# Kernel tuning notes

Hardware: AMD Instinct MI355X
Metric: run time of the kernel (lower is better)

Reference implementation:

```python
import jax, jax.numpy as jnp
import numpy as np

B, T, IN = 64, 1024, 512
H1, H2 = 64, 6

def _mk(key, shape, scale):
    return jax.random.uniform(key, shape, jnp.float32, -scale, scale)

def setup_inputs() -> dict:
    key = jax.random.key(0)
    ks = jax.random.split(key, 16)
    x = jax.random.normal(ks[0], (B, T, IN), jnp.float32)
    s1 = 1.0 / np.sqrt(H1)
    s2 = 1.0 / np.sqrt(H2)
    return {
        "x": x,
        # lstm1 (input 512 -> 64), 2 layers; bias = b_ih + b_hh folded together
        "w1_ih0": _mk(ks[1], (4 * H1, IN), s1), "w1_hh0": _mk(ks[2], (4 * H1, H1), s1), "b1_0": _mk(ks[3], (4 * H1,), s1),
        "w1_ih1": _mk(ks[4], (4 * H1, H1), s1), "w1_hh1": _mk(ks[5], (4 * H1, H1), s1), "b1_1": _mk(ks[6], (4 * H1,), s1),
        # lstm2 (64 -> 6), 2 layers
        "w2_ih0": _mk(ks[7], (4 * H2, H1), s2), "w2_hh0": _mk(ks[8], (4 * H2, H2), s2), "b2_0": _mk(ks[9], (4 * H2,), s2),
        "w2_ih1": _mk(ks[10], (4 * H2, H2), s2), "w2_hh1": _mk(ks[11], (4 * H2, H2), s2), "b2_1": _mk(ks[12], (4 * H2,), s2),
        # fc 6 -> 6
        "fc_w": _mk(ks[13], (H2, H2), s2), "fc_b": _mk(ks[14], (H2,), s2),
    }

def _lstm_layer(x, w_ih, w_hh, b):
    # x: [B, T, D]; w_ih: [4H, D]; w_hh: [4H, H]; b: [4H]
    H = w_hh.shape[1]
    xg = jnp.einsum('btd,gd->btg', x, w_ih) + b          # precompute input gates [B,T,4H]
    xg = jnp.transpose(xg, (1, 0, 2))                    # [T, B, 4H]
    h0 = jnp.zeros((x.shape[0], H), x.dtype)
    c0 = jnp.zeros((x.shape[0], H), x.dtype)

    def step(carry, g_t):
        h, c = carry
        gates = g_t + h @ w_hh.T                         # [B, 4H]
        i, f, g, o = jnp.split(gates, 4, axis=-1)        # pytorch gate order i,f,g,o
        i = jax.nn.sigmoid(i); f = jax.nn.sigmoid(f)
        g = jnp.tanh(g); o = jax.nn.sigmoid(o)
        c = f * c + i * g
        h = o * jnp.tanh(c)
        return (h, c), h

    _, hs = jax.lax.scan(step, (h0, c0), xg)             # hs: [T, B, H]
    return jnp.transpose(hs, (1, 0, 2))                  # [B, T, H]

def reference(x, w1_ih0, w1_hh0, b1_0, w1_ih1, w1_hh1, b1_1,
              w2_ih0, w2_hh0, b2_0, w2_ih1, w2_hh1, b2_1, fc_w, fc_b):
    h = _lstm_layer(x, w1_ih0, w1_hh0, b1_0)
    h = _lstm_layer(h, w1_ih1, w1_hh1, b1_1)
    h = _lstm_layer(h, w2_ih0, w2_hh0, b2_0)
    h = _lstm_layer(h, w2_ih1, w2_hh1, b2_1)
    return h @ fc_w.T + fc_b                             # [B, T, 6]
```

## Files before the change

kernel.cpp:

```cpp
#include <hip/hip_runtime.h>
#include <hip/hip_bf16.h>


#define B_SZ 64
#define T_SZ 1024
#define M_SZ (B_SZ * T_SZ)
#define CHUNK 16
#define PF 4

typedef _Float16 h2   __attribute__((ext_vector_type(2)));
typedef _Float16 h8   __attribute__((ext_vector_type(8)));
typedef float    f32x4 __attribute__((ext_vector_type(4)));

__device__ __forceinline__ float sigm_f(float x) {
    return 1.0f / (1.0f + __expf(-x));
}
__device__ __forceinline__ float tanh_f(float x) {
    return 2.0f / (1.0f + __expf(-2.0f * x)) - 1.0f;
}

__device__ __forceinline__ float fdot2f(h2 a, h2 b, float c) {
#if __has_builtin(__builtin_amdgcn_fdot2)
    return __builtin_amdgcn_fdot2(a, b, c, false);
#else
    return c + (float)a.x * (float)b.x + (float)a.y * (float)b.y;
#endif
}

__device__ __forceinline__ unsigned pack_h2(float a, float b) {
    h2 p; p.x = (_Float16)a; p.y = (_Float16)b;
    return __builtin_bit_cast(unsigned, p);
}
__device__ __forceinline__ h2 as_h2(unsigned x) { return __builtin_bit_cast(h2, x); }
__device__ __forceinline__ float as_f(unsigned x) { return __builtin_bit_cast(float, x); }
__device__ __forceinline__ float as_f(int x) { return __builtin_bit_cast(float, x); }

__device__ __forceinline__ int pack_pair(float h) {
    const _Float16 hf = (_Float16)h;
    const int hb = (int)__builtin_bit_cast(unsigned short, hf);
    const int nb = __builtin_amdgcn_update_dpp(0, hb, 0xB1, 0xF, 0xF, true);
    return hb | (nb << 16);
}

__device__ __forceinline__ void lstm_cell(float p0, float p1, float p2, float p3,
                                          float& c, float& h) {
    const float iv = sigm_f(p0);
    const float fv = sigm_f(p1);
    const float gv = tanh_f(p2);
    const float ov = sigm_f(p3);
    c = fv * c + iv * gv;
    h = ov * tanh_f(c);
}

__device__ __forceinline__ void wait_flag(const unsigned* f, unsigned need) {
    while (__hip_atomic_load(f, __ATOMIC_RELAXED, __HIP_MEMORY_SCOPE_AGENT) < need)
        __builtin_amdgcn_s_sleep(2);
    (void)__hip_atomic_load(f, __ATOMIC_ACQUIRE, __HIP_MEMORY_SCOPE_AGENT);
}
__device__ __forceinline__ void publish_flag(unsigned* f, unsigned v) {
    __hip_atomic_store(f, v, __ATOMIC_RELEASE, __HIP_MEMORY_SCOPE_AGENT);
}

__global__ __launch_bounds__(256) void f32_to_f16(const float* __restrict__ src,
                                                  _Float16* __restrict__ dst, int n) {
    const int i = blockIdx.x * 256 + threadIdx.x;
    if (i < n) dst[i] = (_Float16)src[i];
}

__global__ void init_flags(unsigned* f) { f[threadIdx.x] = 0; }

template <int K>
__global__ __launch_bounds__(256) void gemm_mfma(const float* __restrict__ X,
                                                 const _Float16* __restrict__ W16,
                                                 const float* __restrict__ bias,
                                                 float* __restrict__ out) {
    const int m0   = blockIdx.x * 64;
    const int tid  = threadIdx.x;
    const int wv   = tid >> 6;
    const int lane = tid & 63;
    const int lh   = lane & 15;
    const int quad = lane >> 4;
    const int n0   = wv * 64;

    __shared__ __align__(16) _Float16 Als[64 * 32];

    f32x4 acc[4][4];
#pragma unroll
    for (int nt = 0; nt < 4; ++nt) {
        const float bg = bias[n0 + nt * 16 + lh];
#pragma unroll
        for (int mt = 0; mt < 4; ++mt) {
            acc[mt][nt].x = bg; acc[mt][nt].y = bg;
            acc[mt][nt].z = bg; acc[mt][nt].w = bg;
        }
    }

    const int srow = tid >> 2;
    const int sk8  = tid & 3;
    const int sdst = srow * 32 + ((sk8 ^ (srow & 3)) * 8);

    for (int k0 = 0; k0 < K; k0 += 32) {
        const float* xr = X + (size_t)(m0 + srow) * K + k0 + sk8 * 8;
        const float4 a4 = ((const float4*)xr)[0];
        const float4 b4 = ((const float4*)xr)[1];
        h8 bfrag[4];
#pragma unroll
        for (int nt = 0; nt < 4; ++nt) {
            bfrag[nt] = *(const h8*)&W16[(size_t)(n0 + nt * 16 + lh) * K + k0 + quad * 8];
        }
        h8 hv;
        hv[0] = (_Float16)a4.x; hv[1] = (_Float16)a4.y;
        hv[2] = (_Float16)a4.z; hv[3] = (_Float16)a4.w;
        hv[4] = (_Float16)b4.x; hv[5] = (_Float16)b4.y;
        hv[6] = (_Float16)b4.z; hv[7] = (_Float16)b4.w;

        __syncthreads();
        *(h8*)&Als[sdst] = hv;
        __syncthreads();

        h8 afrag[4];
#pragma unroll
        for (int mt = 0; mt < 4; ++mt) {
            const int row = mt * 16 + lh;
            afrag[mt] = *(const h8*)&Als[row * 32 + ((quad ^ (row & 3)) * 8)];
        }
#pragma unroll
        for (int mt = 0; mt < 4; ++mt)
#pragma unroll
            for (int nt = 0; nt < 4; ++nt)
                acc[mt][nt] = __builtin_amdgcn_mfma_f32_16x16x32_f16(
                    afrag[mt], bfrag[nt], acc[mt][nt], 0, 0, 0);
    }

#pragma unroll
    for (int mt = 0; mt < 4; ++mt)
#pragma unroll
        for (int nt = 0; nt < 4; ++nt)
#pragma unroll
            for (int r = 0; r < 4; ++r)
                out[(size_t)(m0 + mt * 16 + quad * 4 + r) * 256 + n0 + nt * 16 + lh] =
                    acc[mt][nt][r];
}

__global__ __launch_bounds__(256, 1) void lstm_pipe(
        const float* __restrict__ xg,
        const float* __restrict__ whh1,
        const float* __restrict__ wih2,
        const float* __restrict__ whh2,
        const float* __restrict__ b2v,
        const float* __restrict__ wih3,
        const float* __restrict__ whh3,
        const float* __restrict__ b3v,
        const float* __restrict__ wih4,
        const float* __restrict__ whh4,
        const float* __restrict__ b4v,
        const float* __restrict__ fcw,
        const float* __restrict__ fcb,
        unsigned* __restrict__ h1p,
        float* __restrict__ h2g,
        unsigned* __restrict__ flags,
        float* __restrict__ out) {
    const int role = blockIdx.x >> 6;
    const int b    = blockIdx.x & 63;
    const int tid  = threadIdx.x;
    const int g    = tid >> 6;
    const int u    = tid & 63;

    __shared__ __align__(16) float pls[2][4][64];

    if (role == 0) {
        unsigned w[32];
        {
            const float* wr = whh1 + (size_t)(g * 64 + u) * 64;
#pragma unroll
            for (int k2 = 0; k2 < 32; ++k2) w[k2] = pack_h2(wr[2 * k2], wr[2 * k2 + 1]);
        }
        const float* xgb = xg + (size_t)b * T_SZ * 256 + g * 64 + u;
        float xv[4];
#pragma unroll
        for (int s = 0; s < 4; ++s) xv[s] = xgb[(size_t)s * 256];
        unsigned* hp = h1p + (size_t)b * T_SZ * 32;
        unsigned* fl = flags + b;
        float c = 0.0f, h = 0.0f;
        int pkS = 0;

        for (int t4 = 0; t4 < T_SZ; t4 += 4) {
#pragma unroll
            for (int s = 0; s < 4; ++s) {
                const int t = t4 + s;
                float a0 = xv[s], a1 = 0.f, a2 = 0.f, a3 = 0.f;
#pragma unroll
                for (int k8 = 0; k8 < 8; ++k8) {
                    const int hs0 = __builtin_amdgcn_readlane(pkS, 8 * k8 + 0);
                    const int hs1 = __builtin_amdgcn_readlane(pkS, 8 * k8 + 2);
                    const int hs2 = __builtin_amdgcn_readlane(pkS, 8 * k8 + 4);
                    const int hs3 = __builtin_amdgcn_readlane(pkS, 8 * k8 + 6);
                    a0 = fdot2f(as_h2(w[4 * k8 + 0]), __builtin_bit_cast(h2, hs0), a0);
                    a1 = fdot2f(as_h2(w[4 * k8 + 1]), __builtin_bit_cast(h2, hs1), a1);
                    a2 = fdot2f(as_h2(w[4 * k8 + 2]), __builtin_bit_cast(h2, hs2), a2);
                    a3 = fdot2f(as_h2(w[4 * k8 + 3]), __builtin_bit_cast(h2, hs3), a3);
                }
                pls[t & 1][g][u] = (a0 + a1) + (a2 + a3);
                asm volatile("s_waitcnt lgkmcnt(0)" ::: "memory");
                __builtin_amdgcn_s_barrier();
                asm volatile("" ::: "memory");
                const float p0 = pls[t & 1][0][u];
                const float p1 = pls[t & 1][1][u];
                const float p2 = pls[t & 1][2][u];
                const float p3 = pls[t & 1][3][u];
                const int tp = (t + 4 < T_SZ) ? (t + 4) : (T_SZ - 1);
                xv[s] = xgb[(size_t)tp * 256];
                lstm_cell(p0, p1, p2, p3, c, h);
                pkS = pack_pair(h);
                if (g == 0) {
                    if (!(u & 1)) hp[(size_t)t * 32 + (u >> 1)] = (unsigned)pkS;
                    if (u == 0 && ((t & (CHUNK - 1)) == (CHUNK - 1)))
                        publish_flag(fl, (unsigned)(t + 1));
                }
            }
        }
    } else if (role == 1) {
        unsigned wi[32], wh[32];
        {
            const float* a = wih2 + (size_t)(g * 64 + u) * 64;
            const float* bb = whh2 + (size_t)(g * 64 + u) * 64;
#pragma unroll
            for (int k2 = 0; k2 < 32; ++k2) {
                wi[k2] = pack_h2(a[2 * k2], a[2 * k2 + 1]);
                wh[k2] = pack_h2(bb[2 * k2], bb[2 * k2 + 1]);
            }
        }
        const float bias = b2v[g * 64 + u];
        const unsigned* hp = h1p + (size_t)b * T_SZ * 32;
        float* h2b = h2g + (size_t)b * T_SZ * 64;
        unsigned* flin  = flags + b;
        unsigned* flout = flags + 64 + b;

        wait_flag(flin, (T_SZ < CHUNK + PF) ? T_SZ : (CHUNK + PF));
        unsigned hv[4];
#pragma unroll
        for (int s = 0; s < 4; ++s) hv[s] = hp[(size_t)s * 32 + (u & 31)];
        float c = 0.0f, h = 0.0f;
        int pkQ = 0;

        for (int t4 = 0; t4 < T_SZ; t4 += 4) {
            if (t4 && (t4 & (CHUNK - 1)) == 0) {
                unsigned need = t4 + CHUNK + PF;
                if (need > T_SZ) need = T_SZ;
                wait_flag(flin, need);
            }
#pragma unroll
            for (int s = 0; s < 4; ++s) {
                const int t = t4 + s;
                const int hw = (int)hv[s];
                float a0 = bias, a1 = 0.f, a2 = 0.f, a3 = 0.f;
                float d0 = 0.f, d1 = 0.f, d2 = 0.f, d3 = 0.f;
#pragma unroll
                for (int k8 = 0; k8 < 8; ++k8) {
                    const int j = 4 * k8;
                    const int i0 = __builtin_amdgcn_readlane(hw, j + 0);
                    const int i1 = __builtin_amdgcn_readlane(hw, j + 1);
                    const int i2 = __builtin_amdgcn_readlane(hw, j + 2);
                    const int i3 = __builtin_amdgcn_readlane(hw, j + 3);
                    a0 = fdot2f(as_h2(wi[j + 0]), __builtin_bit_cast(h2, i0), a0);
                    a1 = fdot2f(as_h2(wi[j + 1]), __builtin_bit_cast(h2, i1), a1);
                    a2 = fdot2f(as_h2(wi[j + 2]), __builtin_bit_cast(h2, i2), a2);
                    a3 = fdot2f(as_h2(wi[j + 3]), __builtin_bit_cast(h2, i3), a3);
                    const int q0 = __builtin_amdgcn_readlane(pkQ, 2 * j + 0);
                    const int q1 = __builtin_amdgcn_readlane(pkQ, 2 * j + 2);
                    const int q2 = __builtin_amdgcn_readlane(pkQ, 2 * j + 4);
                    const int q3 = __builtin_amdgcn_readlane(pkQ, 2 * j + 6);
                    d0 = fdot2f(as_h2(wh[j + 0]), __builtin_bit_cast(h2, q0), d0);
                    d1 = fdot2f(as_h2(wh[j + 1]), __builtin_bit_cast(h2, q1), d1);
                    d2 = fdot2f(as_h2(wh[j + 2]), __builtin_bit_cast(h2, q2), d2);
                    d3 = fdot2f(as_h2(wh[j + 3]), __builtin_bit_cast(h2, q3), d3);
                }
                pls[t & 1][g][u] = ((a0 + a1) + (a2 + a3)) + ((d0 + d1) + (d2 + d3));
                asm volatile("s_waitcnt lgkmcnt(0)" ::: "memory");
                __builtin_amdgcn_s_barrier();
                asm volatile("" ::: "memory");
                const float p0 = pls[t & 1][0][u];
                const float p1 = pls[t & 1][1][u];
                const float p2 = pls[t & 1][2][u];
                const float p3 = pls[t & 1][3][u];
                const int tp = (t + 4 < T_SZ) ? (t + 4) : (T_SZ - 1);
                hv[s] = hp[(size_t)tp * 32 + (u & 31)];
                lstm_cell(p0, p1, p2, p3, c, h);
                pkQ = pack_pair(h);
                if (g == 0) {
                    h2b[(size_t)t * 64 + u] = h;
                    if (u == 0 && ((t & (CHUNK - 1)) == (CHUNK - 1)))
                        publish_flag(flout, (unsigned)(t + 1));
                }
            }
        }
    } else {
        if (tid >= 64) return;
        float pw[64];
#pragma unroll
        for (int i = 0; i < 64; ++i) pw[i] = 0.0f;
        float pb = 0.0f;

        if (u < 6) {
#pragma unroll
            for (int g4 = 0; g4 < 4; ++g4)
#pragma unroll
                for (int k = 0; k < 6; ++k)
                    pw[g4 * 6 + k] = whh3[(g4 * 6 + u) * 6 + k];
        } else if (u < 12) {
            const int q = u - 6;
#pragma unroll
            for (int g4 = 0; g4 < 4; ++g4) {
#pragma unroll
                for (int k = 0; k < 6; ++k) {
                    pw[g4 * 6 + k]      = wih4[(g4 * 6 + q) * 6 + k];
                    pw[24 + g4 * 6 + k] = whh4[(g4 * 6 + q) * 6 + k];
                }
                pw[48 + g4] = b4v[g4 * 6 + q];
            }
        } else if (u < 18) {
            const int q = u - 12;
#pragma unroll
            for (int k = 0; k < 6; ++k) pw[52 + k] = fcw[q * 6 + k];
            pb = fcb[q];
        } else if (u >= 24 && u < 48) {
            const int q = u - 24;
#pragma unroll
            for (int j = 0; j < 64; ++j) pw[j] = wih3[(size_t)q * 64 + j];
            pb = b3v[q];
        }

        const float* h2b = h2g + (size_t)b * T_SZ * 64;
        unsigned* flin = flags + 64 + b;
        float* outb = out + (size_t)b * T_SZ * 6;

        wait_flag(flin, (T_SZ < CHUNK + PF) ? T_SZ : (CHUNK + PF));
        float hv[4];
#pragma unroll
        for (int s = 0; s < 4; ++s) hv[s] = h2b[(size_t)s * 64 + u];
        float c = 0.0f, h = 0.0f;
        const int bpa = 96 + (u % 6) * 4;

        for (int t4 = 0; t4 < T_SZ + 4; t4 += 4) {
            if (t4 && t4 < T_SZ && (t4 & (CHUNK - 1)) == 0) {
                unsigned need = t4 + CHUNK + PF;
                if (need > T_SZ) need = T_SZ;
                wait_flag(flin, need);
            }
#pragma unroll
            for (int s = 0; s < 4; ++s) {
                const int tt = t4 + s;
                const int hb = __builtin_bit_cast(int, h);
                float v3[6], v4[6];
#pragma unroll
                for (int k = 0; k < 6; ++k) v3[k] = as_f(__builtin_amdgcn_readlane(hb, k));
#pragma unroll
                for (int k = 0; k < 6; ++k) v4[k] = as_f(__builtin_amdgcn_readlane(hb, 6 + k));

                if (tt >= 2 && tt < T_SZ + 2 && u >= 12 && u < 18) {
                    float o = pb;
#pragma unroll
                    for (int k = 0; k < 6; ++k) o = fmaf(pw[52 + k], v4[k], o);
                    outb[(size_t)(tt - 2) * 6 + (u - 12)] = o;
                }
                if (tt >= 1 && tt <= T_SZ && u >= 6 && u < 12) {
                    float pg0 = pw[48], pg1 = pw[49], pg2 = pw[50], pg3 = pw[51];
#pragma unroll
                    for (int k = 0; k < 6; ++k) {
                        pg0 = fmaf(pw[0 * 6 + k], v3[k], pg0);
                        pg1 = fmaf(pw[1 * 6 + k], v3[k], pg1);
                        pg2 = fmaf(pw[2 * 6 + k], v3[k], pg2);
                        pg3 = fmaf(pw[3 * 6 + k], v3[k], pg3);
                        pg0 = fmaf(pw[24 + 0 * 6 + k], v4[k], pg0);
                        pg1 = fmaf(pw[24 + 1 * 6 + k], v4[k], pg1);
                        pg2 = fmaf(pw[24 + 2 * 6 + k], v4[k], pg2);
                        pg3 = fmaf(pw[24 + 3 * 6 + k], v4[k], pg3);
                    }
                    lstm_cell(pg0, pg1, pg2, pg3, c, h);
                }
                float pr = 0.0f;
                if (tt < T_SZ) {
                    const int hw = __builtin_bit_cast(int, hv[s]);
                    float d0 = pb, d1 = 0.f, d2 = 0.f, d3 = 0.f;
#pragma unroll
                    for (int j = 0; j < 64; j += 4) {
                        d0 = fmaf(pw[j + 0], as_f(__builtin_amdgcn_readlane(hw, j + 0)), d0);
                        d1 = fmaf(pw[j + 1], as_f(__builtin_amdgcn_readlane(hw, j + 1)), d1);
                        d2 = fmaf(pw[j + 2], as_f(__builtin_amdgcn_readlane(hw, j + 2)), d2);
                        d3 = fmaf(pw[j + 3], as_f(__builtin_amdgcn_readlane(hw, j + 3)), d3);
                    }
                    pr = (d0 + d1) + (d2 + d3);
                }
                const int prb = __builtin_bit_cast(int, pr);
                float pr4[4];
#pragma unroll
                for (int g4 = 0; g4 < 4; ++g4)
                    pr4[g4] = as_f(__builtin_amdgcn_ds_bpermute(bpa + g4 * 24, prb));
                if (tt < T_SZ) {
                    const int tp = (tt + 4 < T_SZ) ? (tt + 4) : (T_SZ - 1);
                    hv[s] = h2b[(size_t)tp * 64 + u];
                }
                if (tt < T_SZ && u < 6) {
                    float q0 = pr4[0], q1 = pr4[1], q2 = pr4[2], q3 = pr4[3];
#pragma unroll
                    for (int k = 0; k < 6; ++k) {
                        q0 = fmaf(pw[0 * 6 + k], v3[k], q0);
                        q1 = fmaf(pw[1 * 6 + k], v3[k], q1);
                        q2 = fmaf(pw[2 * 6 + k], v3[k], q2);
                        q3 = fmaf(pw[3 * 6 + k], v3[k], q3);
                    }
                    lstm_cell(q0, q1, q2, q3, c, h);
                }
            }
        }
    }
}

extern "C" void kernel_launch(void* const* d_in, const int* in_sizes, int n_in,
                              void* d_out, int out_size, void* d_ws, size_t ws_size,
                              hipStream_t stream) {
    const float* x      = (const float*)d_in[0];
    const float* w1_ih0 = (const float*)d_in[1];
    const float* w1_hh0 = (const float*)d_in[2];
    const float* b1_0   = (const float*)d_in[3];
    const float* w1_ih1 = (const float*)d_in[4];
    const float* w1_hh1 = (const float*)d_in[5];
    const float* b1_1   = (const float*)d_in[6];
    const float* w2_ih0 = (const float*)d_in[7];
    const float* w2_hh0 = (const float*)d_in[8];
    const float* b2_0   = (const float*)d_in[9];
    const float* w2_ih1 = (const float*)d_in[10];
    const float* w2_hh1 = (const float*)d_in[11];
    const float* b2_1   = (const float*)d_in[12];
    const float* fc_w   = (const float*)d_in[13];
    const float* fc_b   = (const float*)d_in[14];
    float* out = (float*)d_out;

    const int M = M_SZ;
    float*    xg    = (float*)d_ws;
    unsigned* h1p   = (unsigned*)(xg + (size_t)M * 256);
    float*    h2g   = (float*)(h1p + (size_t)M * 32);
    _Float16* w16a  = (_Float16*)(h2g + (size_t)M * 64);
    unsigned* flags = (unsigned*)(w16a + 256 * 512);

    init_flags<<<1, 128, 0, stream>>>(flags);
    f32_to_f16<<<(256 * 512 + 255) / 256, 256, 0, stream>>>(w1_ih0, w16a, 256 * 512);

    gemm_mfma<512><<<M / 64, 256, 0, stream>>>(x, w16a, b1_0, xg);

    lstm_pipe<<<192, 256, 0, stream>>>(xg, w1_hh0,
                                       w1_ih1, w1_hh1, b1_1,
                                       w2_ih0, w2_hh0, b2_0,
                                       w2_ih1, w2_hh1, b2_1,
                                       fc_w, fc_b,
                                       h1p, h2g, flags, out);
}
```

Before: 1.154 ms.

## Split LSTM input projections into separate pipelined block roles

The fused recurrent kernel is reorganized from three roles into five. Dedicated blocks now compute the layer-2 and layer-3 input projections chunk by chunk and hand them on through flags, with layer 2 writing in place into the already-consumed xg buffer and layer 3 using a new pr3 buffer. This takes the input matvecs off the serial per-timestep recurrence of the layer-2 and tail-layer blocks, so each recurrent step only does the hidden-state product. The cost is more blocks (320 instead of 192), which must all be co-resident for the spin-waits to work, plus extra global traffic and one more flag handoff adding pipeline latency.

```diff
diff --git a/kernel.cpp b/kernel.cpp
--- a/kernel.cpp
+++ b/kernel.cpp
@@ -143,7 +143,8 @@
 }
 
 __global__ __launch_bounds__(256, 1) void lstm_pipe(
-        const float* __restrict__ xg,
+        const float* __restrict__ xgc,
+        float* __restrict__ xgw,
         const float* __restrict__ whh1,
         const float* __restrict__ wih2,
         const float* __restrict__ whh2,
@@ -158,6 +159,7 @@
         const float* __restrict__ fcb,
         unsigned* __restrict__ h1p,
         float* __restrict__ h2g,
+        float* __restrict__ pr3,
         unsigned* __restrict__ flags,
         float* __restrict__ out) {
     const int role = blockIdx.x >> 6;
@@ -175,7 +177,7 @@
 #pragma unroll
             for (int k2 = 0; k2 < 32; ++k2) w[k2] = pack_h2(wr[2 * k2], wr[2 * k2 + 1]);
         }
-        const float* xgb = xg + (size_t)b * T_SZ * 256 + g * 64 + u;
+        const float* xgb = xgc + (size_t)b * T_SZ * 256 + g * 64 + u;
         float xv[4];
 #pragma unroll
         for (int s = 0; s < 4; ++s) xv[s] = xgb[(size_t)s * 256];
@@ -220,26 +222,61 @@
             }
         }
     } else if (role == 1) {
-        unsigned wi[32], wh[32];
+        unsigned wi[32];
         {
             const float* a = wih2 + (size_t)(g * 64 + u) * 64;
-            const float* bb = whh2 + (size_t)(g * 64 + u) * 64;
-#pragma unroll
-            for (int k2 = 0; k2 < 32; ++k2) {
-                wi[k2] = pack_h2(a[2 * k2], a[2 * k2 + 1]);
-                wh[k2] = pack_h2(bb[2 * k2], bb[2 * k2 + 1]);
-            }
-        }
-        const float bias = b2v[g * 64 + u];
+#pragma unroll
+            for (int k2 = 0; k2 < 32; ++k2) wi[k2] = pack_h2(a[2 * k2], a[2 * k2 + 1]);
+        }
+        const float breg = b2v[g * 64 + u];
         const unsigned* hp = h1p + (size_t)b * T_SZ * 32;
+        float* p2 = xgw + (size_t)b * T_SZ * 256 + g * 64 + u;
+        unsigned* fin  = flags + b;
+        unsigned* fout = flags + 64 + b;
+
+        for (int c0 = 0; c0 < T_SZ; c0 += CHUNK) {
+            wait_flag(fin, (unsigned)(c0 + CHUNK));
+            for (int tt = c0; tt < c0 + CHUNK; tt += 4) {
+                unsigned hv[4];
+#pragma unroll
+                for (int s = 0; s < 4; ++s) hv[s] = hp[(size_t)(tt + s) * 32 + (u & 31)];
+#pragma unroll
+                for (int s = 0; s < 4; ++s) {
+                    const int hw = (int)hv[s];
+                    float a0 = breg, a1 = 0.f, a2 = 0.f, a3 = 0.f;
+#pragma unroll
+                    for (int k8 = 0; k8 < 8; ++k8) {
+                        const int j = 4 * k8;
+                        const int i0 = __builtin_amdgcn_readlane(hw, j + 0);
+                        const int i1 = __builtin_amdgcn_readlane(hw, j + 1);
+                        const int i2 = __builtin_amdgcn_readlane(hw, j + 2);
+                        const int i3 = __builtin_amdgcn_readlane(hw, j + 3);
+                        a0 = fdot2f(as_h2(wi[j + 0]), __builtin_bit_cast(h2, i0), a0);
+                        a1 = fdot2f(as_h2(wi[j + 1]), __builtin_bit_cast(h2, i1), a1);
+                        a2 = fdot2f(as_h2(wi[j + 2]), __builtin_bit_cast(h2, i2), a2);
+                        a3 = fdot2f(as_h2(wi[j + 3]), __builtin_bit_cast(h2, i3), a3);
+                    }
+                    p2[(size_t)(tt + s) * 256] = (a0 + a1) + (a2 + a3);
+                }
+            }
+            publish_flag(fout, (unsigned)(c0 + CHUNK));
+        }
+    } else if (role == 2) {
+        unsigned wh[32];
+        {
+            const float* a = whh2 + (size_t)(g * 64 + u) * 64;
+#pragma unroll
+            for (int k2 = 0; k2 < 32; ++k2) wh[k2] = pack_h2(a[2 * k2], a[2 * k2 + 1]);
+        }
+        const float* p2 = xgc + (size_t)b * T_SZ * 256 + g * 64 + u;
         float* h2b = h2g + (size_t)b * T_SZ * 64;
-        unsigned* flin  = flags + b;
-        unsigned* flout = flags + 64 + b;
-
-        wait_flag(flin, (T_SZ < CHUNK + PF) ? T_SZ : (CHUNK + PF));
-        unsigned hv[4];
-#pragma unroll
-        for (int s = 0; s < 4; ++s) hv[s] = hp[(size_t)s * 32 + (u & 31)];
+        unsigned* fin  = flags + 64 + b;
+        unsigned* fout = flags + 128 + b;
+
+        wait_flag(fin, (T_SZ < CHUNK + PF) ? T_SZ : (CHUNK + PF));
+        float xv[4];
+#pragma unroll
+        for (int s = 0; s < 4; ++s) xv[s] = p2[(size_t)s * 256];
         float c = 0.0f, h = 0.0f;
         int pkQ = 0;
 
@@ -247,141 +284,68 @@
             if (t4 && (t4 & (CHUNK - 1)) == 0) {
                 unsigned need = t4 + CHUNK + PF;
                 if (need > T_SZ) need = T_SZ;
-                wait_flag(flin, need);
+                wait_flag(fin, need);
             }
 #pragma unroll
             for (int s = 0; s < 4; ++s) {
                 const int t = t4 + s;
-                const int hw = (int)hv[s];
-                float a0 = bias, a1 = 0.f, a2 = 0.f, a3 = 0.f;
-                float d0 = 0.f, d1 = 0.f, d2 = 0.f, d3 = 0.f;
+                float a0 = xv[s], a1 = 0.f, a2 = 0.f, a3 = 0.f;
 #pragma unroll
                 for (int k8 = 0; k8 < 8; ++k8) {
-                    const int j = 4 * k8;
-                    const int i0 = __builtin_amdgcn_readlane(hw, j + 0);
-                    const int i1 = __builtin_amdgcn_readlane(hw, j + 1);
-                    const int i2 = __builtin_amdgcn_readlane(hw, j + 2);
-                    const int i3 = __builtin_amdgcn_readlane(hw, j + 3);
-                    a0 = fdot2f(as_h2(wi[j + 0]), __builtin_bit_cast(h2, i0), a0);
-                    a1 = fdot2f(as_h2(wi[j + 1]), __builtin_bit_cast(h2, i1), a1);
-                    a2 = fdot2f(as_h2(wi[j + 2]), __builtin_bit_cast(h2, i2), a2);
-                    a3 = fdot2f(as_h2(wi[j + 3]), __builtin_bit_cast(h2, i3), a3);
-                    const int q0 = __builtin_amdgcn_readlane(pkQ, 2 * j + 0);
-                    const int q1 = __builtin_amdgcn_readlane(pkQ, 2 * j + 2);
-                    const int q2 = __builtin_amdgcn_readlane(pkQ, 2 * j + 4);
-                    const int q3 = __builtin_amdgcn_readlane(pkQ, 2 * j + 6);
-                    d0 = fdot2f(as_h2(wh[j + 0]), __builtin_bit_cast(h2, q0), d0);
-                    d1 = fdot2f(as_h2(wh[j + 1]), __builtin_bit_cast(h2, q1), d1);
-                    d2 = fdot2f(as_h2(wh[j + 2]), __builtin_bit_cast(h2, q2), d2);
-                    d3 = fdot2f(as_h2(wh[j + 3]), __builtin_bit_cast(h2, q3), d3);
-                }
-                pls[t & 1][g][u] = ((a0 + a1) + (a2 + a3)) + ((d0 + d1) + (d2 + d3));
+                    const int q0 = __builtin_amdgcn_readlane(pkQ, 8 * k8 + 0);
+                    const int q1 = __builtin_amdgcn_readlane(pkQ, 8 * k8 + 2);
+                    const int q2 = __builtin_amdgcn_readlane(pkQ, 8 * k8 + 4);
+                    const int q3 = __builtin_amdgcn_readlane(pkQ, 8 * k8 + 6);
+                    a0 = fdot2f(as_h2(wh[4 * k8 + 0]), __builtin_bit_cast(h2, q0), a0);
+                    a1 = fdot2f(as_h2(wh[4 * k8 + 1]), __builtin_bit_cast(h2, q1), a1);
+                    a2 = fdot2f(as_h2(wh[4 * k8 + 2]), __builtin_bit_cast(h2, q2), a2);
+                    a3 = fdot2f(as_h2(wh[4 * k8 + 3]), __builtin_bit_cast(h2, q3), a3);
+                }
+                pls[t & 1][g][u] = (a0 + a1) + (a2 + a3);
                 asm volatile("s_waitcnt lgkmcnt(0)" ::: "memory");
                 __builtin_amdgcn_s_barrier();
                 asm volatile("" ::: "memory");
                 const float p0 = pls[t & 1][0][u];
                 const float p1 = pls[t & 1][1][u];
-                const float p2 = pls[t & 1][2][u];
+                const float p2v = pls[t & 1][2][u];
                 const float p3 = pls[t & 1][3][u];
                 const int tp = (t + 4 < T_SZ) ? (t + 4) : (T_SZ - 1);
-                hv[s] = hp[(size_t)tp * 32 + (u & 31)];
-                lstm_cell(p0, p1, p2, p3, c, h);
+                xv[s] = p2[(size_t)tp * 256];
+                lstm_cell(p0, p1, p2v, p3, c, h);
                 pkQ = pack_pair(h);
                 if (g == 0) {
                     h2b[(size_t)t * 64 + u] = h;
                     if (u == 0 && ((t & (CHUNK - 1)) == (CHUNK - 1)))
-                        publish_flag(flout, (unsigned)(t + 1));
-                }
-            }
-        }
-    } else {
+                        publish_flag(fout, (unsigned)(t + 1));
+                }
+            }
+        }
+    } else if (role == 3) {
         if (tid >= 64) return;
         float pw[64];
 #pragma unroll
-        for (int i = 0; i < 64; ++i) pw[i] = 0.0f;
-        float pb = 0.0f;
-
-        if (u < 6) {
-#pragma unroll
-            for (int g4 = 0; g4 < 4; ++g4)
-#pragma unroll
-                for (int k = 0; k < 6; ++k)
-                    pw[g4 * 6 + k] = whh3[(g4 * 6 + u) * 6 + k];
-        } else if (u < 12) {
-            const int q = u - 6;
-#pragma unroll
-            for (int g4 = 0; g4 < 4; ++g4) {
-#pragma unroll
-                for (int k = 0; k < 6; ++k) {
-                    pw[g4 * 6 + k]      = wih4[(g4 * 6 + q) * 6 + k];
-                    pw[24 + g4 * 6 + k] = whh4[(g4 * 6 + q) * 6 + k];
-                }
-                pw[48 + g4] = b4v[g4 * 6 + q];
-            }
-        } else if (u < 18) {
-            const int q = u - 12;
-#pragma unroll
-            for (int k = 0; k < 6; ++k) pw[52 + k] = fcw[q * 6 + k];
-            pb = fcb[q];
-        } else if (u >= 24 && u < 48) {
-            const int q = u - 24;
-#pragma unroll
-            for (int j = 0; j < 64; ++j) pw[j] = wih3[(size_t)q * 64 + j];
-            pb = b3v[q];
-        }
-
+        for (int j = 0; j < 64; ++j) pw[j] = 0.0f;
+        float breg = 0.0f;
+        if (u < 24) {
+#pragma unroll
+            for (int j = 0; j < 64; ++j) pw[j] = wih3[(size_t)u * 64 + j];
+            breg = b3v[u];
+        }
         const float* h2b = h2g + (size_t)b * T_SZ * 64;
-        unsigned* flin = flags + 64 + b;
-        float* outb = out + (size_t)b * T_SZ * 6;
-
-        wait_flag(flin, (T_SZ < CHUNK + PF) ? T_SZ : (CHUNK + PF));
-        float hv[4];
-#pragma unroll
-        for (int s = 0; s < 4; ++s) hv[s] = h2b[(size_t)s * 64 + u];
-        float c = 0.0f, h = 0.0f;
-        const int bpa = 96 + (u % 6) * 4;
-
-        for (int t4 = 0; t4 < T_SZ + 4; t4 += 4) {
-            if (t4 && t4 < T_SZ && (t4 & (CHUNK - 1)) == 0) {
-                unsigned need = t4 + CHUNK + PF;
-                if (need > T_SZ) need = T_SZ;
-                wait_flag(flin, need);
-            }
-#pragma unroll
-            for (int s = 0; s < 4; ++s) {
-                const int tt = t4 + s;
-                const int hb = __builtin_bit_cast(int, h);
-                float v3[6], v4[6];
-#pragma unroll
-                for (int k = 0; k < 6; ++k) v3[k] = as_f(__builtin_amdgcn_readlane(hb, k));
-#pragma unroll
-                for (int k = 0; k < 6; ++k) v4[k] = as_f(__builtin_amdgcn_readlane(hb, 6 + k));
-
-                if (tt >= 2 && tt < T_SZ + 2 && u >= 12 && u < 18) {
-                    float o = pb;
-#pragma unroll
-                    for (int k = 0; k < 6; ++k) o = fmaf(pw[52 + k], v4[k], o);
-                    outb[(size_t)(tt - 2) * 6 + (u - 12)] = o;
-                }
-                if (tt >= 1 && tt <= T_SZ && u >= 6 && u < 12) {
-                    float pg0 = pw[48], pg1 = pw[49], pg2 = pw[50], pg3 = pw[51];
-#pragma unroll
-                    for (int k = 0; k < 6; ++k) {
-                        pg0 = fmaf(pw[0 * 6 + k], v3[k], pg0);
-                        pg1 = fmaf(pw[1 * 6 + k], v3[k], pg1);
-                        pg2 = fmaf(pw[2 * 6 + k], v3[k], pg2);
-                        pg3 = fmaf(pw[3 * 6 + k], v3[k], pg3);
-                        pg0 = fmaf(pw[24 + 0 * 6 + k], v4[k], pg0);
-                        pg1 = fmaf(pw[24 + 1 * 6 + k], v4[k], pg1);
-                        pg2 = fmaf(pw[24 + 2 * 6 + k], v4[k], pg2);
-                        pg3 = fmaf(pw[24 + 3 * 6 + k], v4[k], pg3);
-                    }
-                    lstm_cell(pg0, pg1, pg2, pg3, c, h);
-                }
-                float pr = 0.0f;
-                if (tt < T_SZ) {
+        float* prb = pr3 + (size_t)b * T_SZ * 24;
+        unsigned* fin  = flags + 128 + b;
+        unsigned* fout = flags + 192 + b;
+
+        for (int c0 = 0; c0 < T_SZ; c0 += CHUNK) {
+            wait_flag(fin, (unsigned)(c0 + CHUNK));
+            for (int tt = c0; tt < c0 + CHUNK; tt += 4) {
+                float hv[4];
+#pragma unroll
+                for (int s = 0; s < 4; ++s) hv[s] = h2b[(size_t)(tt + s) * 64 + u];
+#pragma unroll
+                for (int s = 0; s < 4; ++s) {
                     const int hw = __builtin_bit_cast(int, hv[s]);
-                    float d0 = pb, d1 = 0.f, d2 = 0.f, d3 = 0.f;
+                    float d0 = breg, d1 = 0.f, d2 = 0.f, d3 = 0.f;
 #pragma unroll
                     for (int j = 0; j < 64; j += 4) {
                         d0 = fmaf(pw[j + 0], as_f(__builtin_amdgcn_readlane(hw, j + 0)), d0);
@@ -389,28 +353,95 @@
                         d2 = fmaf(pw[j + 2], as_f(__builtin_amdgcn_readlane(hw, j + 2)), d2);
                         d3 = fmaf(pw[j + 3], as_f(__builtin_amdgcn_readlane(hw, j + 3)), d3);
                     }
-                    pr = (d0 + d1) + (d2 + d3);
-                }
-                const int prb = __builtin_bit_cast(int, pr);
-                float pr4[4];
-#pragma unroll
-                for (int g4 = 0; g4 < 4; ++g4)
-                    pr4[g4] = as_f(__builtin_amdgcn_ds_bpermute(bpa + g4 * 24, prb));
-                if (tt < T_SZ) {
-                    const int tp = (tt + 4 < T_SZ) ? (tt + 4) : (T_SZ - 1);
-                    hv[s] = h2b[(size_t)tp * 64 + u];
-                }
-                if (tt < T_SZ && u < 6) {
-                    float q0 = pr4[0], q1 = pr4[1], q2 = pr4[2], q3 = pr4[3];
-#pragma unroll
-                    for (int k = 0; k < 6; ++k) {
-                        q0 = fmaf(pw[0 * 6 + k], v3[k], q0);
-                        q1 = fmaf(pw[1 * 6 + k], v3[k], q1);
-                        q2 = fmaf(pw[2 * 6 + k], v3[k], q2);
-                        q3 = fmaf(pw[3 * 6 + k], v3[k], q3);
-                    }
-                    lstm_cell(q0, q1, q2, q3, c, h);
-                }
+                    if (u < 24) prb[(size_t)(tt + s) * 24 + u] = (d0 + d1) + (d2 + d3);
+                }
+            }
+            publish_flag(fout, (unsigned)(c0 + CHUNK));
+        }
+    } else {
+        if (tid >= 64) return;
+        float pw[48];
+#pragma unroll
+        for (int j = 0; j < 48; ++j) pw[j] = 0.0f;
+        float wf[7] = {0.f, 0.f, 0.f, 0.f, 0.f, 0.f, 0.f};
+        float wb[4] = {0.f, 0.f, 0.f, 0.f};
+        if (u < 6) {
+#pragma unroll
+            for (int g4 = 0; g4 < 4; ++g4)
+#pragma unroll
+                for (int k = 0; k < 6; ++k)
+                    pw[g4 * 12 + k] = whh3[(g4 * 6 + u) * 6 + k];
+        } else if (u < 12) {
+            const int q = u - 6;
+#pragma unroll
+            for (int g4 = 0; g4 < 4; ++g4) {
+#pragma unroll
+                for (int k = 0; k < 6; ++k) {
+                    pw[g4 * 12 + k]     = wih4[(g4 * 6 + q) * 6 + k];
+                    pw[g4 * 12 + 6 + k] = whh4[(g4 * 6 + q) * 6 + k];
+                }
+                wb[g4] = b4v[g4 * 6 + q];
+            }
+        } else if (u < 18) {
+            const int q = u - 12;
+#pragma unroll
+            for (int k = 0; k < 6; ++k) wf[k] = fcw[q * 6 + k];
+            wf[6] = fcb[q];
+        }
+        const float* prb = pr3 + (size_t)b * T_SZ * 24;
+        float* outb = out + (size_t)b * T_SZ * 6;
+        unsigned* fin = flags + 192 + b;
+        const int up  = (u < 24) ? u : 23;
+        const int bpa = ((u % 6) * 4);
+
+        wait_flag(fin, (T_SZ < CHUNK + PF) ? T_SZ : (CHUNK + PF));
+        float pf[4];
+#pragma unroll
+        for (int s = 0; s < 4; ++s) pf[s] = prb[(size_t)s * 24 + up];
+        float hS = 0.0f, cS = 0.0f;
+
+        for (int t4 = 0; t4 < T_SZ + 4; t4 += 4) {
+            if (t4 && t4 < T_SZ && (t4 & (CHUNK - 1)) == 0) {
+                unsigned need = t4 + CHUNK + PF;
+                if (need > T_SZ) need = T_SZ;
+                wait_flag(fin, need);
+            }
+#pragma unroll
+            for (int s = 0; s < 4; ++s) {
+                const int t = t4 + s;
+                const int hb = __builtin_bit_cast(int, hS);
+                float v[12];
+#pragma unroll
+                for (int k = 0; k < 12; ++k)
+                    v[k] = as_f(__builtin_amdgcn_readlane(hb, k));
+                if (t >= 2 && t < T_SZ + 2 && u >= 12 && u < 18) {
+                    float o = wf[6];
+#pragma unroll
+                    for (int k = 0; k < 6; ++k) o = fmaf(wf[k], v[6 + k], o);
+                    outb[(size_t)(t - 2) * 6 + (u - 12)] = o;
+                }
+                float pj[4];
+                {
+                    const int prbits = __builtin_bit_cast(int, pf[s]);
+#pragma unroll
+                    for (int g4 = 0; g4 < 4; ++g4)
+                        pj[g4] = as_f(__builtin_amdgcn_ds_bpermute(bpa + g4 * 24, prbits));
+                }
+                {
+                    const int tp = (t + 4 < T_SZ) ? (t + 4) : (T_SZ - 1);
+                    pf[s] = prb[(size_t)tp * 24 + up];
+                }
+                const bool is_l4 = (u >= 6 && u < 12);
+                float pg[4];
+#pragma unroll
+                for (int g4 = 0; g4 < 4; ++g4) {
+                    float a = is_l4 ? wb[g4] : pj[g4];
+#pragma unroll
+                    for (int k = 0; k < 12; ++k) a = fmaf(pw[g4 * 12 + k], v[k], a);
+                    pg[g4] = a;
+                }
+                const bool act = (u < 6 && t < T_SZ) || (is_l4 && t >= 1 && t <= T_SZ);
+                if (act) lstm_cell(pg[0], pg[1], pg[2], pg[3], cS, hS);
             }
         }
     }
@@ -440,18 +471,19 @@
     float*    xg    = (float*)d_ws;
     unsigned* h1p   = (unsigned*)(xg + (size_t)M * 256);
     float*    h2g   = (float*)(h1p + (size_t)M * 32);
-    _Float16* w16a  = (_Float16*)(h2g + (size_t)M * 64);
+    float*    pr3   = h2g + (size_t)M * 64;
+    _Float16* w16a  = (_Float16*)(pr3 + (size_t)M * 24);
     unsigned* flags = (unsigned*)(w16a + 256 * 512);
 
-    init_flags<<<1, 128, 0, stream>>>(flags);
+    init_flags<<<1, 256, 0, stream>>>(flags);
     f32_to_f16<<<(256 * 512 + 255) / 256, 256, 0, stream>>>(w1_ih0, w16a, 256 * 512);
 
     gemm_mfma<512><<<M / 64, 256, 0, stream>>>(x, w16a, b1_0, xg);
 
-    lstm_pipe<<<192, 256, 0, stream>>>(xg, w1_hh0,
+    lstm_pipe<<<320, 256, 0, stream>>>(xg, xg, w1_hh0,
                                        w1_ih1, w1_hh1, b1_1,
                                        w2_ih0, w2_hh0, b2_0,
                                        w2_ih1, w2_hh1, b2_1,
                                        fc_w, fc_b,
-                                       h1p, h2g, flags, out);
-}
+                                       h1p, h2g, pr3, flags, out);
+}
```

Measured after the change: 1.344 ms. 16.4% more time.
